# Optimization experiments

Measured on AMD Instinct MI355X. Metric: run time of the kernel, lower is better.

Reference implementation:

```python
import jax, jax.numpy as jnp
import numpy as np

B, LQ, LK, D = 32, 2048, 2048, 128
MASK_P = 0.1  # fraction of masked-out (True) positions


def setup_inputs() -> dict:
    key = jax.random.key(0)
    kq, kk, kv, km = jax.random.split(key, 4)
    q = jax.random.normal(kq, (B, LQ, D), dtype=jnp.float32)
    k = jax.random.normal(kk, (B, LK, D), dtype=jnp.float32)
    v = jax.random.normal(kv, (B, LK, D), dtype=jnp.float32)
    mask = jax.random.bernoulli(km, MASK_P, (B, LQ, LK))  # True = masked out
    return {"q": q, "k": k, "v": v, "mask": mask}


def reference(q, k, v, mask):
    # Faithful to the original: score is MULTIPLIED by sqrt(dk) (module's bug kept).
    dk = k.shape[-1]
    score = jnp.einsum('bqd,bkd->bqk', q, k) * jnp.sqrt(jnp.float32(dk))
    # masked_fill_(mask, -inf)
    score = jnp.where(mask, -jnp.inf, score)
    attn = jax.nn.softmax(score, axis=2)
    # torch.where(isnan(attn), 0, attn): fully-masked rows (all -inf) -> 0
    attn = jnp.where(jnp.isnan(attn), jnp.zeros_like(attn), attn)
    # dropout_rate = 0.0 -> identity
    context = jnp.einsum('bqk,bkd->bqd', attn, v)
    return context
```

## Files before the change

### kernel.cpp

```cpp
#include <hip/hip_runtime.h>
#include <math.h>

#define NB  32
#define NLQ 2048
#define NLK 2048
#define ND  128
#define KT  64
#define SCALE2 16.3231239813435843f
#define SCALE  11.3137084989847603904f

typedef float f32x4 __attribute__((ext_vector_type(4)));
typedef short s16x8 __attribute__((ext_vector_type(8)));
typedef unsigned short u16;
typedef unsigned short u16x8 __attribute__((ext_vector_type(8)));
typedef unsigned long long u64;

__device__ int g_maskflag;

static __device__ __forceinline__ u16 f2bf(float x) {
    unsigned int u = __float_as_uint(x);
    return (u16)((u + 0x7FFFu + ((u >> 16) & 1u)) >> 16);
}
static __device__ __forceinline__ float bf2f(u16 b) {
    return __uint_as_float(((unsigned int)b) << 16);
}

#define SPLIT8(H, L, J, VAL) do { float _v = (VAL); u16 _hb = f2bf(_v); \
    (H)[J] = (short)_hb; (L)[J] = (short)f2bf(_v - bf2f(_hb)); } while (0)

#define GLDS(lds, src) __builtin_amdgcn_global_load_lds( \
    (const __attribute__((address_space(1))) unsigned int*)(src), \
    (__attribute__((address_space(3))) unsigned int*)(lds), 16, 0, 0)

__global__ void zero_flag_kernel() { if (threadIdx.x == 0) g_maskflag = 0; }

__global__ void detect_mask_kernel(const unsigned char* __restrict__ m) {
    unsigned int i = blockIdx.x * blockDim.x + threadIdx.x;
    bool nz = m[(size_t)i * 4 + 1] != 0;
    if (__any((int)nz) && (threadIdx.x & 63) == 0) atomicOr(&g_maskflag, 1);
}

__global__ void __launch_bounds__(256)
maskbits_kernel(const unsigned char* __restrict__ M, u64* __restrict__ Bits) {
    const size_t NWORDS = (size_t)NB * NLQ * (NLK / 64);
    const int ln = threadIdx.x & 63;
    const size_t wgid = ((size_t)blockIdx.x * 256 + threadIdx.x) >> 6;
    const size_t NW = (size_t)4096 * 4;
    if (g_maskflag != 0) {
        #pragma unroll 4
        for (size_t w = wgid; w < NWORDS; w += NW) {
            unsigned char v = M[w * 64 + ln];
            u64 bal = __ballot(v != 0);
            if (ln == 0) Bits[w] = bal;
        }
    } else {
        const int* Mi = (const int*)M;
        #pragma unroll 4
        for (size_t w = wgid; w < NWORDS; w += NW) {
            int v = Mi[w * 64 + ln];
            u64 bal = __ballot(v != 0);
            if (ln == 0) Bits[w] = bal;
        }
    }
}

__global__ void __launch_bounds__(256)
ksplit_kernel(const float* __restrict__ K, u16* __restrict__ Khi, u16* __restrict__ Klo) {
    int idx  = blockIdx.x * 256 + threadIdx.x;
    int d0   = (idx & 15) << 3;
    int krow = idx >> 4;
    const float* src = K + (size_t)krow * ND + d0;
    float4 x0 = *(const float4*)src;
    float4 x1 = *(const float4*)(src + 4);
    float xs[8] = {x0.x, x0.y, x0.z, x0.w, x1.x, x1.y, x1.z, x1.w};
    u16x8 h, l;
    #pragma unroll
    for (int j = 0; j < 8; ++j) { u16 hb = f2bf(xs[j]); h[j] = hb; l[j] = f2bf(xs[j] - bf2f(hb)); }
    int kkl = krow & 63;
    size_t tbase = ((size_t)(krow >> 6)) * 8192;
    int off = (kkl * ND + d0) ^ ((kkl & 7) << 3);
    *(u16x8*)(Khi + tbase + off) = h;
    *(u16x8*)(Klo + tbase + off) = l;
}

__global__ void __launch_bounds__(256)
vtrans_kernel(const float* __restrict__ V, u16* __restrict__ Vt) {
    int gw = (blockIdx.x * 256 + threadIdx.x) >> 6;
    int ln = threadIdx.x & 63;
    int dgrp = gw & 15;
    int tile = gw >> 4;
    int dl = ln >> 3, chunk = ln & 7;
    int d = dgrp * 8 + dl;
    int kk0 = chunk * 8;
    const float* src = V + ((size_t)tile * 64 + kk0) * ND + d;
    u16x8 o;
    #pragma unroll
    for (int j = 0; j < 8; ++j) o[j] = f2bf(src[(size_t)j * ND]);
    *(u16x8*)(Vt + (size_t)tile * 8192 + ((d * KT + kk0) ^ ((d & 7) << 3))) = o;
}

__global__ void __launch_bounds__(512, 2)
attn3_kernel(const float* __restrict__ Q, const u64* __restrict__ Bits,
             float* __restrict__ Out,
             const u16* __restrict__ Khi, const u16* __restrict__ Klo,
             const u16* __restrict__ Vt)
{
    extern __shared__ u16 smem[];
    u16* bufA = smem;
    u16* bufB = smem + 24576;
    u16* sPb  = smem + 49152;

    const int tid  = threadIdx.x;
    const int wave = tid >> 6;
    const int ln   = tid & 63;
    const int g    = ln >> 4;
    const int qi   = ln & 15;

    const int n    = blockIdx.x;
    const int orig = ((n & 7) << 5) | (n >> 3);
    const int b    = orig >> 3;
    const int qt   = orig & 7;
    const int qbase = qt * 256 + wave * 32;

    s16x8 qh8[2][4], ql8[2][4];
    #pragma unroll
    for (int u = 0; u < 2; ++u) {
        const float* qp = Q + ((size_t)b * NLQ + qbase + u * 16 + qi) * ND;
        #pragma unroll
        for (int c = 0; c < 4; ++c) {
            const float* p = qp + c * 32 + g * 8;
            float4 x0 = *(const float4*)(p);
            float4 x1 = *(const float4*)(p + 4);
            s16x8 h, l;
            SPLIT8(h, l, 0, x0.x * SCALE2); SPLIT8(h, l, 1, x0.y * SCALE2);
            SPLIT8(h, l, 2, x0.z * SCALE2); SPLIT8(h, l, 3, x0.w * SCALE2);
            SPLIT8(h, l, 4, x1.x * SCALE2); SPLIT8(h, l, 5, x1.y * SCALE2);
            SPLIT8(h, l, 6, x1.z * SCALE2); SPLIT8(h, l, 7, x1.w * SCALE2);
            qh8[u][c] = h; ql8[u][c] = l;
        }
    }

    f32x4 o[2][8];
    #pragma unroll
    for (int u = 0; u < 2; ++u)
        #pragma unroll
        for (int t = 0; t < 8; ++t) o[u][t] = (f32x4){0.f, 0.f, 0.f, 0.f};
    float mrun[2] = {-INFINITY, -INFINITY}, lsum[2] = {0.f, 0.f};

    const u16* khT = Khi + (size_t)b * 32 * 8192;
    const u16* klT = Klo + (size_t)b * 32 * 8192;
    const u16* vtT = Vt  + (size_t)b * 32 * 8192;

    const size_t row0 = (size_t)b * NLQ + qbase + qi;
    const u64* bw0 = Bits + row0 * 32;
    const u64* bw1 = Bits + (row0 + 16) * 32;

#define STAGE_TILE(dst, kt_) do { \
    const char* _sK = (const char*)(khT + (size_t)(kt_) * 8192) + wave * 2048 + ln * 16; \
    const char* _sL = (const char*)(klT + (size_t)(kt_) * 8192) + wave * 2048 + ln * 16; \
    const char* _sV = (const char*)(vtT + (size_t)(kt_) * 8192) + wave * 2048 + ln * 16; \
    GLDS((dst) + wave * 1024,               _sK); \
    GLDS((dst) + wave * 1024 + 512,         _sK + 1024); \
    GLDS((dst) + 8192  + wave * 1024,       _sL); \
    GLDS((dst) + 8192  + wave * 1024 + 512, _sL + 1024); \
    GLDS((dst) + 16384 + wave * 1024,       _sV); \
    GLDS((dst) + 16384 + wave * 1024 + 512, _sV + 1024); \
} while (0)

    STAGE_TILE(bufA, 0);
    u64 mw0 = bw0[0], mw1 = bw1[0];
    __syncthreads();

    u16* cur = bufA;
    u16* nxt = bufB;

    for (int kt = 0; kt < 32; ++kt) {
        u64 nmw0 = mw0, nmw1 = mw1;
        if (kt < 31) {
            STAGE_TILE(nxt, kt + 1);
            nmw0 = bw0[kt + 1];
            nmw1 = bw1[kt + 1];
        }

        u16* sKh = cur;
        u16* sKl = cur + 8192;
        u16* sVt_ = cur + 16384;

        float p[2][16];
        #pragma unroll
        for (int s = 0; s < 4; ++s) {
            f32x4 a0 = (f32x4){0.f, 0.f, 0.f, 0.f};
            f32x4 a1 = (f32x4){0.f, 0.f, 0.f, 0.f};
            int row = s * 16 + qi;
            int rowoff = row * ND, swz = (row & 7) << 3;
            #pragma unroll
            for (int c = 0; c < 4; ++c) {
                int off = (rowoff + c * 32 + g * 8) ^ swz;
                s16x8 kh = *(s16x8*)&sKh[off];
                s16x8 kl = *(s16x8*)&sKl[off];
                a0 = __builtin_amdgcn_mfma_f32_16x16x32_bf16(kh, qh8[0][c], a0, 0, 0, 0);
                a1 = __builtin_amdgcn_mfma_f32_16x16x32_bf16(kh, qh8[1][c], a1, 0, 0, 0);
                a0 = __builtin_amdgcn_mfma_f32_16x16x32_bf16(kh, ql8[0][c], a0, 0, 0, 0);
                a1 = __builtin_amdgcn_mfma_f32_16x16x32_bf16(kh, ql8[1][c], a1, 0, 0, 0);
                a0 = __builtin_amdgcn_mfma_f32_16x16x32_bf16(kl, qh8[0][c], a0, 0, 0, 0);
                a1 = __builtin_amdgcn_mfma_f32_16x16x32_bf16(kl, qh8[1][c], a1, 0, 0, 0);
            }
            #pragma unroll
            for (int r = 0; r < 4; ++r) { p[0][s * 4 + r] = a0[r]; p[1][s * 4 + r] = a1[r]; }
        }

        #pragma unroll
        for (int u = 0; u < 2; ++u) {
            u64 mw = u ? mw1 : mw0;
            unsigned mbits = 0;
            #pragma unroll
            for (int s = 0; s < 4; ++s)
                mbits |= (unsigned)((mw >> (s * 16 + 4 * g)) & 0xFull) << (4 * s);

            float tm = -INFINITY;
            #pragma unroll
            for (int i = 0; i < 16; ++i) {
                float sv = ((mbits >> i) & 1u) ? -INFINITY : p[u][i];
                p[u][i] = sv;
                tm = fmaxf(tm, sv);
            }
            tm = fmaxf(tm, __shfl_xor(tm, 16));
            tm = fmaxf(tm, __shfl_xor(tm, 32));

            float mold = mrun[u];
            bool defer = (mold > -INFINITY) && __all((int)(tm <= mold + 8.f));
            float m_use = mold;
            if (!defer) {
                float mnew = fmaxf(mold, tm);
                float corr = (mnew == -INFINITY) ? 0.f : __builtin_exp2f(mold - mnew);
                lsum[u] *= corr;
                #pragma unroll
                for (int j = 0; j < 4; ++j) {
                    float cj = __shfl(corr, 4 * g + j, 64);
                    #pragma unroll
                    for (int t = 0; t < 8; ++t) o[u][t][j] *= cj;
                }
                mrun[u] = mnew;
                m_use = mnew;
            }

            float psum = 0.f;
            #pragma unroll
            for (int i = 0; i < 16; ++i) {
                float pv = ((mbits >> i) & 1u) ? 0.f : __builtin_exp2f(p[u][i] - m_use);
                p[u][i] = pv;
                psum += pv;
            }
            psum += __shfl_xor(psum, 16);
            psum += __shfl_xor(psum, 32);
            lsum[u] += psum;

            u16* sP = sPb + (wave * 2 + u) * 1024;
            #pragma unroll
            for (int s = 0; s < 4; ++s) {
                ushort4 p4;
                p4.x = f2bf(p[u][s * 4 + 0]); p4.y = f2bf(p[u][s * 4 + 1]);
                p4.z = f2bf(p[u][s * 4 + 2]); p4.w = f2bf(p[u][s * 4 + 3]);
                int off = (qi * KT + s * 16 + 4 * g) ^ ((qi & 7) << 3);
                *(ushort4*)&sP[off] = p4;
            }
        }

        u16* sP0 = sPb + (wave * 2 + 0) * 1024;
        u16* sP1 = sPb + (wave * 2 + 1) * 1024;
        #pragma unroll
        for (int h = 0; h < 2; ++h) {
            int offp = (qi * KT + h * 32 + g * 8) ^ ((qi & 7) << 3);
            s16x8 pa0 = *(s16x8*)&sP0[offp];
            s16x8 pa1 = *(s16x8*)&sP1[offp];
            #pragma unroll
            for (int t = 0; t < 8; ++t) {
                int d = t * 16 + qi;
                int offv = (d * KT + h * 32 + g * 8) ^ ((d & 7) << 3);
                s16x8 vb = *(s16x8*)&sVt_[offv];
                o[0][t] = __builtin_amdgcn_mfma_f32_16x16x32_bf16(pa0, vb, o[0][t], 0, 0, 0);
                o[1][t] = __builtin_amdgcn_mfma_f32_16x16x32_bf16(pa1, vb, o[1][t], 0, 0, 0);
            }
        }

        __syncthreads();
        mw0 = nmw0; mw1 = nmw1;
        u16* tswap = cur; cur = nxt; nxt = tswap;
    }

    #pragma unroll
    for (int u = 0; u < 2; ++u)
        #pragma unroll
        for (int j = 0; j < 4; ++j) {
            float lj = __shfl(lsum[u], 4 * g + j, 64);
            float inv = (lj > 0.f) ? (1.0f / lj) : 0.f;
            int row = qbase + u * 16 + 4 * g + j;
            float* op = Out + ((size_t)b * NLQ + row) * ND + qi;
            #pragma unroll
            for (int t = 0; t < 8; ++t) op[t * 16] = o[u][t][j] * inv;
        }
#undef STAGE_TILE
}

__global__ void __launch_bounds__(256, 2)
attn_fallback(const float* __restrict__ Q, const float* __restrict__ K,
              const float* __restrict__ V, const unsigned char* __restrict__ Mb,
              float* __restrict__ Out)
{
    __shared__ u16 sKh[KT * ND];
    __shared__ u16 sKl[KT * ND];
    __shared__ u16 sVt[ND * KT];
    __shared__ u16 sP[4][16 * KT];

    const int tid  = threadIdx.x;
    const int wave = tid >> 6;
    const int ln   = tid & 63;
    const int g    = ln >> 4;
    const int qi   = ln & 15;

    const int bid   = blockIdx.x;
    const int b     = bid >> 5;
    const int qt    = bid & 31;
    const int qbase = qt * 64;
    const int qrow  = qbase + wave * 16 + qi;

    const bool maskByte = (g_maskflag != 0);

    s16x8 qh8[4], ql8[4];
    {
        const float* qp = Q + ((size_t)b * NLQ + qrow) * ND;
        #pragma unroll
        for (int c = 0; c < 4; ++c) {
            const float* p = qp + c * 32 + g * 8;
            float4 x0 = *(const float4*)(p);
            float4 x1 = *(const float4*)(p + 4);
            s16x8 h, l;
            SPLIT8(h, l, 0, x0.x * SCALE); SPLIT8(h, l, 1, x0.y * SCALE);
            SPLIT8(h, l, 2, x0.z * SCALE); SPLIT8(h, l, 3, x0.w * SCALE);
            SPLIT8(h, l, 4, x1.x * SCALE); SPLIT8(h, l, 5, x1.y * SCALE);
            SPLIT8(h, l, 6, x1.z * SCALE); SPLIT8(h, l, 7, x1.w * SCALE);
            qh8[c] = h; ql8[c] = l;
        }
    }

    f32x4 o[8];
    #pragma unroll
    for (int t = 0; t < 8; ++t) o[t] = (f32x4){0.f, 0.f, 0.f, 0.f};
    float m_run = -INFINITY, lsumv = 0.f;

    const float* kbp = K + (size_t)b * NLK * ND;
    const float* vbp = V + (size_t)b * NLK * ND;
    const size_t mrow = ((size_t)b * NLQ + qrow) * (size_t)NLK;

    for (int kt = 0; kt < NLK / KT; ++kt) {
        const int kb = kt * KT;
        __syncthreads();

        #pragma unroll
        for (int r = 0; r < 8; ++r) {
            int idx = r * 256 + tid;
            int kk  = idx >> 5;
            int d0  = (idx & 31) << 2;
            float4 x = *(const float4*)(kbp + (size_t)(kb + kk) * ND + d0);
            ushort4 h4, l4; u16 hb;
            hb = f2bf(x.x); h4.x = hb; l4.x = f2bf(x.x - bf2f(hb));
            hb = f2bf(x.y); h4.y = hb; l4.y = f2bf(x.y - bf2f(hb));
            hb = f2bf(x.z); h4.z = hb; l4.z = f2bf(x.z - bf2f(hb));
            hb = f2bf(x.w); h4.w = hb; l4.w = f2bf(x.w - bf2f(hb));
            int off = (kk * ND + d0) ^ ((kk & 7) << 3);
            *(ushort4*)&sKh[off] = h4;
            *(ushort4*)&sKl[off] = l4;
        }
        #pragma unroll
        for (int r = 0; r < 2; ++r) {
            int idx = r * 256 + tid;
            int kk0 = (idx >> 5) << 2;
            int d0  = (idx & 31) << 2;
            const float* vp = vbp + (size_t)(kb + kk0) * ND + d0;
            float4 r0 = *(const float4*)(vp);
            float4 r1 = *(const float4*)(vp + ND);
            float4 r2 = *(const float4*)(vp + 2 * ND);
            float4 r3 = *(const float4*)(vp + 3 * ND);
            ushort4 cv;
            cv.x = f2bf(r0.x); cv.y = f2bf(r1.x); cv.z = f2bf(r2.x); cv.w = f2bf(r3.x);
            { int d = d0;     *(ushort4*)&sVt[(d * KT + kk0) ^ ((d & 7) << 3)] = cv; }
            cv.x = f2bf(r0.y); cv.y = f2bf(r1.y); cv.z = f2bf(r2.y); cv.w = f2bf(r3.y);
            { int d = d0 + 1; *(ushort4*)&sVt[(d * KT + kk0) ^ ((d & 7) << 3)] = cv; }
            cv.x = f2bf(r0.z); cv.y = f2bf(r1.z); cv.z = f2bf(r2.z); cv.w = f2bf(r3.z);
            { int d = d0 + 2; *(ushort4*)&sVt[(d * KT + kk0) ^ ((d & 7) << 3)] = cv; }
            cv.x = f2bf(r0.w); cv.y = f2bf(r1.w); cv.z = f2bf(r2.w); cv.w = f2bf(r3.w);
            { int d = d0 + 3; *(ushort4*)&sVt[(d * KT + kk0) ^ ((d & 7) << 3)] = cv; }
        }
        __syncthreads();

        unsigned maskbits = 0;
        if (maskByte) {
            #pragma unroll
            for (int s = 0; s < 4; ++s) {
                unsigned mm = *(const unsigned int*)(Mb + mrow + (size_t)(kb + s * 16 + 4 * g));
                #pragma unroll
                for (int j = 0; j < 4; ++j)
                    maskbits |= (((mm >> (8 * j)) & 0xFFu) ? 1u : 0u) << (s * 4 + j);
            }
        } else {
            const int* Mi = (const int*)Mb;
            #pragma unroll
            for (int s = 0; s < 4; ++s) {
                int4 mm = *(const int4*)(Mi + mrow + (size_t)(kb + s * 16 + 4 * g));
                if (mm.x) maskbits |= 1u << (s * 4 + 0);
                if (mm.y) maskbits |= 1u << (s * 4 + 1);
                if (mm.z) maskbits |= 1u << (s * 4 + 2);
                if (mm.w) maskbits |= 1u << (s * 4 + 3);
            }
        }

        float p[16];
        #pragma unroll
        for (int s = 0; s < 4; ++s) {
            f32x4 acc = (f32x4){0.f, 0.f, 0.f, 0.f};
            int rowoff = (s * 16 + qi) * ND;
            int swz = ((s * 16 + qi) & 7) << 3;
            #pragma unroll
            for (int c = 0; c < 4; ++c) {
                int off = (rowoff + c * 32 + g * 8) ^ swz;
                s16x8 kh = *(s16x8*)&sKh[off];
                s16x8 kl = *(s16x8*)&sKl[off];
                acc = __builtin_amdgcn_mfma_f32_16x16x32_bf16(kh, qh8[c], acc, 0, 0, 0);
                acc = __builtin_amdgcn_mfma_f32_16x16x32_bf16(kh, ql8[c], acc, 0, 0, 0);
                acc = __builtin_amdgcn_mfma_f32_16x16x32_bf16(kl, qh8[c], acc, 0, 0, 0);
            }
            p[s * 4 + 0] = acc[0]; p[s * 4 + 1] = acc[1];
            p[s * 4 + 2] = acc[2]; p[s * 4 + 3] = acc[3];
        }

        float tmax = -INFINITY;
        #pragma unroll
        for (int i = 0; i < 16; ++i) {
            float sv = ((maskbits >> i) & 1u) ? -INFINITY : p[i];
            p[i] = sv;
            tmax = fmaxf(tmax, sv);
        }
        tmax = fmaxf(tmax, __shfl_xor(tmax, 16));
        tmax = fmaxf(tmax, __shfl_xor(tmax, 32));
        float mnew = fmaxf(m_run, tmax);
        float corr = (mnew == -INFINITY) ? 0.f : __expf(m_run - mnew);
        float psum = 0.f;
        #pragma unroll
        for (int i = 0; i < 16; ++i) {
            float pv = ((maskbits >> i) & 1u) ? 0.f : __expf(p[i] - mnew);
            p[i] = pv;
            psum += pv;
        }
        psum += __shfl_xor(psum, 16);
        psum += __shfl_xor(psum, 32);
        lsumv = lsumv * corr + psum;
        m_run = mnew;

        #pragma unroll
        for (int j = 0; j < 4; ++j) {
            float cj = __shfl(corr, 4 * g + j, 64);
            #pragma unroll
            for (int t = 0; t < 8; ++t) o[t][j] *= cj;
        }

        #pragma unroll
        for (int s = 0; s < 4; ++s) {
            ushort4 p4;
            p4.x = f2bf(p[s * 4 + 0]); p4.y = f2bf(p[s * 4 + 1]);
            p4.z = f2bf(p[s * 4 + 2]); p4.w = f2bf(p[s * 4 + 3]);
            int off = (qi * KT + s * 16 + 4 * g) ^ ((qi & 7) << 3);
            *(ushort4*)&sP[wave][off] = p4;
        }
        #pragma unroll
        for (int h = 0; h < 2; ++h) {
            int offp = (qi * KT + h * 32 + g * 8) ^ ((qi & 7) << 3);
            s16x8 pa = *(s16x8*)&sP[wave][offp];
            #pragma unroll
            for (int t = 0; t < 8; ++t) {
                int d = t * 16 + qi;
                int offv = (d * KT + h * 32 + g * 8) ^ ((d & 7) << 3);
                s16x8 vb = *(s16x8*)&sVt[offv];
                o[t] = __builtin_amdgcn_mfma_f32_16x16x32_bf16(pa, vb, o[t], 0, 0, 0);
            }
        }
    }

    #pragma unroll
    for (int j = 0; j < 4; ++j) {
        float lj = __shfl(lsumv, 4 * g + j, 64);
        float inv = (lj > 0.f) ? (1.0f / lj) : 0.f;
        int row = qbase + wave * 16 + 4 * g + j;
        float* op = Out + ((size_t)b * NLQ + row) * ND + qi;
        #pragma unroll
        for (int t = 0; t < 8; ++t) op[t * 16] = o[t][j] * inv;
    }
}

extern "C" void kernel_launch(void* const* d_in, const int* in_sizes, int n_in,
                              void* d_out, int out_size, void* d_ws, size_t ws_size,
                              hipStream_t stream) {
    (void)in_sizes; (void)n_in; (void)out_size;
    const float* Q = (const float*)d_in[0];
    const float* K = (const float*)d_in[1];
    const float* V = (const float*)d_in[2];
    const unsigned char* M = (const unsigned char*)d_in[3];
    float* Out = (float*)d_out;

    zero_flag_kernel<<<1, 64, 0, stream>>>();
    detect_mask_kernel<<<64, 256, 0, stream>>>(M);

    const size_t WS_NEED = (size_t)64 * 1024 * 1024;
    if (ws_size >= WS_NEED) {
        u16* Khi = (u16*)d_ws;
        u16* Klo = Khi + 8388608;
        u16* Vt  = Klo + 8388608;
        u64* Bits = (u64*)(Vt + 8388608);
        maskbits_kernel<<<4096, 256, 0, stream>>>(M, Bits);
        ksplit_kernel<<<4096, 256, 0, stream>>>(K, Khi, Klo);
        vtrans_kernel<<<4096, 256, 0, stream>>>(V, Vt);
        hipFuncSetAttribute((const void*)attn3_kernel,
                            hipFuncAttributeMaxDynamicSharedMemorySize, 131072);
        attn3_kernel<<<256, 512, 131072, stream>>>(Q, Bits, Out, Khi, Klo, Vt);
    } else {
        attn_fallback<<<1024, 256, 0, stream>>>(Q, K, V, M, Out);
    }
}
```

Baseline: 964.2 us.

## Fuse prep kernels and deepen attention pipeline with LDS-staged mask bits

Merges the mask-bit, K split and V transpose kernels into a single prep launch to cut launch overhead. The attention kernel now prefetches two tiles ahead, using raw s_waitcnt/s_barrier instead of __syncthreads, and stages mask words into LDS through global_load_lds. It also interleaves the two softmax halves with the PV MFMAs and adds s_setprio around MFMA blocks to overlap compute with softmax work. Dynamic LDS grows to 144KB, and the hand-written vmcnt counts make the pipeline fragile.

```diff
diff --git a/kernel.cpp b/kernel.cpp
--- a/kernel.cpp
+++ b/kernel.cpp
@@ -41,66 +41,114 @@
 }
 
 __global__ void __launch_bounds__(256)
-maskbits_kernel(const unsigned char* __restrict__ M, u64* __restrict__ Bits) {
-    const size_t NWORDS = (size_t)NB * NLQ * (NLK / 64);
-    const int ln = threadIdx.x & 63;
-    const size_t wgid = ((size_t)blockIdx.x * 256 + threadIdx.x) >> 6;
-    const size_t NW = (size_t)4096 * 4;
-    if (g_maskflag != 0) {
-        #pragma unroll 4
-        for (size_t w = wgid; w < NWORDS; w += NW) {
-            unsigned char v = M[w * 64 + ln];
-            u64 bal = __ballot(v != 0);
-            if (ln == 0) Bits[w] = bal;
-        }
+prep_kernel(const float* __restrict__ K, const float* __restrict__ V,
+            const unsigned char* __restrict__ M,
+            u16* __restrict__ Khi, u16* __restrict__ Klo, u16* __restrict__ Vt,
+            u64* __restrict__ Bits)
+{
+    const int blk = blockIdx.x;
+    if (blk < 4096) {
+        int idx  = blk * 256 + threadIdx.x;
+        int d0   = (idx & 15) << 3;
+        int krow = idx >> 4;
+        const float* src = K + (size_t)krow * ND + d0;
+        float4 x0 = *(const float4*)src;
+        float4 x1 = *(const float4*)(src + 4);
+        float xs[8] = {x0.x, x0.y, x0.z, x0.w, x1.x, x1.y, x1.z, x1.w};
+        u16x8 h, l;
+        #pragma unroll
+        for (int j = 0; j < 8; ++j) { u16 hb = f2bf(xs[j]); h[j] = hb; l[j] = f2bf(xs[j] - bf2f(hb)); }
+        int kkl = krow & 63;
+        size_t tbase = ((size_t)(krow >> 6)) * 8192;
+        int off = (kkl * ND + d0) ^ ((kkl & 7) << 3);
+        *(u16x8*)(Khi + tbase + off) = h;
+        *(u16x8*)(Klo + tbase + off) = l;
+    } else if (blk < 8192) {
+        int gw = ((blk - 4096) * 256 + threadIdx.x) >> 6;
+        int ln = threadIdx.x & 63;
+        int dgrp = gw & 15;
+        int tile = gw >> 4;
+        int dl = ln >> 3, chunk = ln & 7;
+        int d = dgrp * 8 + dl;
+        int kk0 = chunk * 8;
+        const float* src = V + ((size_t)tile * 64 + kk0) * ND + d;
+        u16x8 ov;
+        #pragma unroll
+        for (int j = 0; j < 8; ++j) ov[j] = f2bf(src[(size_t)j * ND]);
+        *(u16x8*)(Vt + (size_t)tile * 8192 + ((d * KT + kk0) ^ ((d & 7) << 3))) = ov;
     } else {
-        const int* Mi = (const int*)M;
-        #pragma unroll 4
-        for (size_t w = wgid; w < NWORDS; w += NW) {
-            int v = Mi[w * 64 + ln];
-            u64 bal = __ballot(v != 0);
-            if (ln == 0) Bits[w] = bal;
-        }
-    }
-}
-
-__global__ void __launch_bounds__(256)
-ksplit_kernel(const float* __restrict__ K, u16* __restrict__ Khi, u16* __restrict__ Klo) {
-    int idx  = blockIdx.x * 256 + threadIdx.x;
-    int d0   = (idx & 15) << 3;
-    int krow = idx >> 4;
-    const float* src = K + (size_t)krow * ND + d0;
-    float4 x0 = *(const float4*)src;
-    float4 x1 = *(const float4*)(src + 4);
-    float xs[8] = {x0.x, x0.y, x0.z, x0.w, x1.x, x1.y, x1.z, x1.w};
-    u16x8 h, l;
-    #pragma unroll
-    for (int j = 0; j < 8; ++j) { u16 hb = f2bf(xs[j]); h[j] = hb; l[j] = f2bf(xs[j] - bf2f(hb)); }
-    int kkl = krow & 63;
-    size_t tbase = ((size_t)(krow >> 6)) * 8192;
-    int off = (kkl * ND + d0) ^ ((kkl & 7) << 3);
-    *(u16x8*)(Khi + tbase + off) = h;
-    *(u16x8*)(Klo + tbase + off) = l;
-}
-
-__global__ void __launch_bounds__(256)
-vtrans_kernel(const float* __restrict__ V, u16* __restrict__ Vt) {
-    int gw = (blockIdx.x * 256 + threadIdx.x) >> 6;
-    int ln = threadIdx.x & 63;
-    int dgrp = gw & 15;
-    int tile = gw >> 4;
-    int dl = ln >> 3, chunk = ln & 7;
-    int d = dgrp * 8 + dl;
-    int kk0 = chunk * 8;
-    const float* src = V + ((size_t)tile * 64 + kk0) * ND + d;
-    u16x8 o;
-    #pragma unroll
-    for (int j = 0; j < 8; ++j) o[j] = f2bf(src[(size_t)j * ND]);
-    *(u16x8*)(Vt + (size_t)tile * 8192 + ((d * KT + kk0) ^ ((d & 7) << 3))) = o;
-}
+        const size_t NWORDS = (size_t)NB * NLQ * (NLK / 64);
+        const int ln = threadIdx.x & 63;
+        const size_t wgid = (((size_t)(blk - 8192)) * 256 + threadIdx.x) >> 6;
+        const size_t NW = (size_t)4096 * 4;
+        if (g_maskflag != 0) {
+            #pragma unroll 4
+            for (size_t w = wgid; w < NWORDS; w += NW) {
+                unsigned char v = M[w * 64 + ln];
+                u64 bal = __ballot(v != 0);
+                if (ln == 0) Bits[w] = bal;
+            }
+        } else {
+            const int* Mi = (const int*)M;
+            #pragma unroll 4
+            for (size_t w = wgid; w < NWORDS; w += NW) {
+                int v = Mi[w * 64 + ln];
+                u64 bal = __ballot(v != 0);
+                if (ln == 0) Bits[w] = bal;
+            }
+        }
+    }
+}
+
+#define SOFTMAX_STORE(MW, P, MRUN, LSUM, OACC, SPTR) do { \
+    unsigned mbits = 0; \
+    _Pragma("unroll") \
+    for (int s = 0; s < 4; ++s) \
+        mbits |= (unsigned)(((MW) >> (s * 16 + 4 * g)) & 0xFull) << (4 * s); \
+    float tm = -INFINITY; \
+    _Pragma("unroll") \
+    for (int i = 0; i < 16; ++i) { \
+        float sv = ((mbits >> i) & 1u) ? -INFINITY : (P)[i]; \
+        (P)[i] = sv; tm = fmaxf(tm, sv); \
+    } \
+    tm = fmaxf(tm, __shfl_xor(tm, 16)); \
+    tm = fmaxf(tm, __shfl_xor(tm, 32)); \
+    float mold = (MRUN); \
+    bool defer = (mold > -INFINITY) && __all((int)(tm <= mold + 8.f)); \
+    float m_use = mold; \
+    if (!defer) { \
+        float mnew = fmaxf(mold, tm); \
+        float corr = (mnew == -INFINITY) ? 0.f : __builtin_exp2f(mold - mnew); \
+        (LSUM) *= corr; \
+        _Pragma("unroll") \
+        for (int j = 0; j < 4; ++j) { \
+            float cj = __shfl(corr, 4 * g + j, 64); \
+            _Pragma("unroll") \
+            for (int t2 = 0; t2 < 8; ++t2) (OACC)[t2][j] *= cj; \
+        } \
+        (MRUN) = mnew; m_use = mnew; \
+    } \
+    float psum = 0.f; \
+    _Pragma("unroll") \
+    for (int i = 0; i < 16; ++i) { \
+        float pv = ((mbits >> i) & 1u) ? 0.f : __builtin_exp2f((P)[i] - m_use); \
+        (P)[i] = pv; psum += pv; \
+    } \
+    psum += __shfl_xor(psum, 16); \
+    psum += __shfl_xor(psum, 32); \
+    (LSUM) += psum; \
+    _Pragma("unroll") \
+    for (int s = 0; s < 4; ++s) { \
+        ushort4 p4; \
+        p4.x = f2bf((P)[s * 4 + 0]); p4.y = f2bf((P)[s * 4 + 1]); \
+        p4.z = f2bf((P)[s * 4 + 2]); p4.w = f2bf((P)[s * 4 + 3]); \
+        int off = (qi * KT + s * 16 + 4 * g) ^ ((qi & 7) << 3); \
+        *(ushort4*)&(SPTR)[off] = p4; \
+    } \
+} while (0)
 
 __global__ void __launch_bounds__(512, 2)
-attn3_kernel(const float* __restrict__ Q, const u64* __restrict__ Bits,
+attn4_kernel(const float* __restrict__ Q, const u64* __restrict__ Bits,
              float* __restrict__ Out,
              const u16* __restrict__ Khi, const u16* __restrict__ Klo,
              const u16* __restrict__ Vt)
@@ -109,6 +157,7 @@
     u16* bufA = smem;
     u16* bufB = smem + 24576;
     u16* sPb  = smem + 49152;
+    char* mbase = (char*)(smem + 65536);
 
     const int tid  = threadIdx.x;
     const int wave = tid >> 6;
@@ -140,20 +189,16 @@
         }
     }
 
-    f32x4 o[2][8];
+    f32x4 o0[8], o1[8];
     #pragma unroll
-    for (int u = 0; u < 2; ++u)
-        #pragma unroll
-        for (int t = 0; t < 8; ++t) o[u][t] = (f32x4){0.f, 0.f, 0.f, 0.f};
-    float mrun[2] = {-INFINITY, -INFINITY}, lsum[2] = {0.f, 0.f};
+    for (int t = 0; t < 8; ++t) { o0[t] = (f32x4){0.f,0.f,0.f,0.f}; o1[t] = (f32x4){0.f,0.f,0.f,0.f}; }
+    float mrun0 = -INFINITY, mrun1 = -INFINITY, lsum0 = 0.f, lsum1 = 0.f;
 
     const u16* khT = Khi + (size_t)b * 32 * 8192;
     const u16* klT = Klo + (size_t)b * 32 * 8192;
     const u16* vtT = Vt  + (size_t)b * 32 * 8192;
-
-    const size_t row0 = (size_t)b * NLQ + qbase + qi;
-    const u64* bw0 = Bits + row0 * 32;
-    const u64* bw1 = Bits + (row0 + 16) * 32;
+    const size_t browbase = (size_t)b * NLQ + qbase;
+    char* mslotw = mbase + wave * 2048;
 
 #define STAGE_TILE(dst, kt_) do { \
     const char* _sK = (const char*)(khT + (size_t)(kt_) * 8192) + wave * 2048 + ln * 16; \
@@ -167,30 +212,40 @@
     GLDS((dst) + 16384 + wave * 1024 + 512, _sV + 1024); \
 } while (0)
 
+#define MASK_STAGE(W_) do { \
+    const char* _sm = (const char*)Bits + ((browbase + (size_t)(ln & 31)) * 32 + (size_t)(W_)) * 8; \
+    GLDS((u16*)(mslotw + (((W_) >> 1) & 1) * 1024), _sm); \
+} while (0)
+
     STAGE_TILE(bufA, 0);
-    u64 mw0 = bw0[0], mw1 = bw1[0];
-    __syncthreads();
-
-    u16* cur = bufA;
-    u16* nxt = bufB;
-
-    for (int kt = 0; kt < 32; ++kt) {
-        u64 nmw0 = mw0, nmw1 = mw1;
-        if (kt < 31) {
-            STAGE_TILE(nxt, kt + 1);
-            nmw0 = bw0[kt + 1];
-            nmw1 = bw1[kt + 1];
-        }
-
-        u16* sKh = cur;
-        u16* sKl = cur + 8192;
-        u16* sVt_ = cur + 16384;
-
-        float p[2][16];
+    MASK_STAGE(0);
+    STAGE_TILE(bufB, 1);
+    MASK_STAGE(2);
+
+    u16* sP0 = sPb + (wave * 2 + 0) * 1024;
+    u16* sP1 = sPb + (wave * 2 + 1) * 1024;
+    const int offp_h0 = (qi * KT + g * 8) ^ ((qi & 7) << 3);
+    const int offp_h1 = (qi * KT + 32 + g * 8) ^ ((qi & 7) << 3);
+
+    for (int t = 0; t < 32; ++t) {
+        u16* cbuf = (t & 1) ? bufB : bufA;
+        u16* sKh = cbuf;
+        u16* sKl = cbuf + 8192;
+        u16* sVt_ = cbuf + 16384;
+
+        asm volatile("s_waitcnt vmcnt(7)" ::: "memory");
+        asm volatile("s_barrier" ::: "memory");
+
+        const char* mbw = mslotw + ((t >> 1) & 1) * 1024 + (t & 1) * 8;
+        u64 mw0 = *(const u64*)(mbw + qi * 16);
+        u64 mw1 = *(const u64*)(mbw + 256 + qi * 16);
+
+        float p0[16], p1[16];
+        __builtin_amdgcn_s_setprio(1);
         #pragma unroll
         for (int s = 0; s < 4; ++s) {
-            f32x4 a0 = (f32x4){0.f, 0.f, 0.f, 0.f};
-            f32x4 a1 = (f32x4){0.f, 0.f, 0.f, 0.f};
+            f32x4 a0 = (f32x4){0.f,0.f,0.f,0.f};
+            f32x4 a1 = (f32x4){0.f,0.f,0.f,0.f};
             int row = s * 16 + qi;
             int rowoff = row * ND, swz = (row & 7) << 3;
             #pragma unroll
@@ -206,100 +261,80 @@
                 a1 = __builtin_amdgcn_mfma_f32_16x16x32_bf16(kl, qh8[1][c], a1, 0, 0, 0);
             }
             #pragma unroll
-            for (int r = 0; r < 4; ++r) { p[0][s * 4 + r] = a0[r]; p[1][s * 4 + r] = a1[r]; }
-        }
-
-        #pragma unroll
-        for (int u = 0; u < 2; ++u) {
-            u64 mw = u ? mw1 : mw0;
-            unsigned mbits = 0;
-            #pragma unroll
-            for (int s = 0; s < 4; ++s)
-                mbits |= (unsigned)((mw >> (s * 16 + 4 * g)) & 0xFull) << (4 * s);
-
-            float tm = -INFINITY;
-            #pragma unroll
-            for (int i = 0; i < 16; ++i) {
-                float sv = ((mbits >> i) & 1u) ? -INFINITY : p[u][i];
-                p[u][i] = sv;
-                tm = fmaxf(tm, sv);
-            }
-            tm = fmaxf(tm, __shfl_xor(tm, 16));
-            tm = fmaxf(tm, __shfl_xor(tm, 32));
-
-            float mold = mrun[u];
-            bool defer = (mold > -INFINITY) && __all((int)(tm <= mold + 8.f));
-            float m_use = mold;
-            if (!defer) {
-                float mnew = fmaxf(mold, tm);
-                float corr = (mnew == -INFINITY) ? 0.f : __builtin_exp2f(mold - mnew);
-                lsum[u] *= corr;
-                #pragma unroll
-                for (int j = 0; j < 4; ++j) {
-                    float cj = __shfl(corr, 4 * g + j, 64);
-                    #pragma unroll
-                    for (int t = 0; t < 8; ++t) o[u][t][j] *= cj;
-                }
-                mrun[u] = mnew;
-                m_use = mnew;
-            }
-
-            float psum = 0.f;
-            #pragma unroll
-            for (int i = 0; i < 16; ++i) {
-                float pv = ((mbits >> i) & 1u) ? 0.f : __builtin_exp2f(p[u][i] - m_use);
-                p[u][i] = pv;
-                psum += pv;
-            }
-            psum += __shfl_xor(psum, 16);
-            psum += __shfl_xor(psum, 32);
-            lsum[u] += psum;
-
-            u16* sP = sPb + (wave * 2 + u) * 1024;
-            #pragma unroll
-            for (int s = 0; s < 4; ++s) {
-                ushort4 p4;
-                p4.x = f2bf(p[u][s * 4 + 0]); p4.y = f2bf(p[u][s * 4 + 1]);
-                p4.z = f2bf(p[u][s * 4 + 2]); p4.w = f2bf(p[u][s * 4 + 3]);
-                int off = (qi * KT + s * 16 + 4 * g) ^ ((qi & 7) << 3);
-                *(ushort4*)&sP[off] = p4;
-            }
-        }
-
-        u16* sP0 = sPb + (wave * 2 + 0) * 1024;
-        u16* sP1 = sPb + (wave * 2 + 1) * 1024;
-        #pragma unroll
-        for (int h = 0; h < 2; ++h) {
-            int offp = (qi * KT + h * 32 + g * 8) ^ ((qi & 7) << 3);
-            s16x8 pa0 = *(s16x8*)&sP0[offp];
-            s16x8 pa1 = *(s16x8*)&sP1[offp];
-            #pragma unroll
-            for (int t = 0; t < 8; ++t) {
-                int d = t * 16 + qi;
-                int offv = (d * KT + h * 32 + g * 8) ^ ((d & 7) << 3);
-                s16x8 vb = *(s16x8*)&sVt_[offv];
-                o[0][t] = __builtin_amdgcn_mfma_f32_16x16x32_bf16(pa0, vb, o[0][t], 0, 0, 0);
-                o[1][t] = __builtin_amdgcn_mfma_f32_16x16x32_bf16(pa1, vb, o[1][t], 0, 0, 0);
-            }
-        }
-
-        __syncthreads();
-        mw0 = nmw0; mw1 = nmw1;
-        u16* tswap = cur; cur = nxt; nxt = tswap;
+            for (int r = 0; r < 4; ++r) { p0[s * 4 + r] = a0[r]; p1[s * 4 + r] = a1[r]; }
+        }
+        __builtin_amdgcn_s_setprio(0);
+
+        SOFTMAX_STORE(mw0, p0, mrun0, lsum0, o0, sP0);
+
+        s16x8 vb[8];
+        #pragma unroll
+        for (int tt = 0; tt < 8; ++tt) {
+            int d = tt * 16 + qi;
+            vb[tt] = *(s16x8*)&sVt_[(d * KT + g * 8) ^ ((d & 7) << 3)];
+        }
+        s16x8 pa00 = *(s16x8*)&sP0[offp_h0];
+        __builtin_amdgcn_s_setprio(1);
+        #pragma unroll
+        for (int tt = 0; tt < 8; ++tt)
+            o0[tt] = __builtin_amdgcn_mfma_f32_16x16x32_bf16(pa00, vb[tt], o0[tt], 0, 0, 0);
+        __builtin_amdgcn_s_setprio(0);
+
+        SOFTMAX_STORE(mw1, p1, mrun1, lsum1, o1, sP1);
+
+        s16x8 pa10 = *(s16x8*)&sP1[offp_h0];
+        __builtin_amdgcn_s_setprio(1);
+        #pragma unroll
+        for (int tt = 0; tt < 8; ++tt)
+            o1[tt] = __builtin_amdgcn_mfma_f32_16x16x32_bf16(pa10, vb[tt], o1[tt], 0, 0, 0);
+        __builtin_amdgcn_s_setprio(0);
+
+        s16x8 pa01 = *(s16x8*)&sP0[offp_h1];
+        s16x8 pa11 = *(s16x8*)&sP1[offp_h1];
+        #pragma unroll
+        for (int tt = 0; tt < 8; ++tt) {
+            int d = tt * 16 + qi;
+            vb[tt] = *(s16x8*)&sVt_[(d * KT + 32 + g * 8) ^ ((d & 7) << 3)];
+        }
+        __builtin_amdgcn_s_setprio(1);
+        #pragma unroll
+        for (int tt = 0; tt < 8; ++tt) {
+            o0[tt] = __builtin_amdgcn_mfma_f32_16x16x32_bf16(pa01, vb[tt], o0[tt], 0, 0, 0);
+            o1[tt] = __builtin_amdgcn_mfma_f32_16x16x32_bf16(pa11, vb[tt], o1[tt], 0, 0, 0);
+        }
+        __builtin_amdgcn_s_setprio(0);
+
+        asm volatile("s_waitcnt lgkmcnt(0)" ::: "memory");
+        asm volatile("s_barrier" ::: "memory");
+
+        if (t < 31) {
+            int nt = t + 2; if (nt > 31) nt = 31;
+            STAGE_TILE(cbuf, nt);
+            int W = nt & ~1; if (W > 30) W = 30;
+            MASK_STAGE(W);
+        }
     }
 
     #pragma unroll
-    for (int u = 0; u < 2; ++u)
-        #pragma unroll
-        for (int j = 0; j < 4; ++j) {
-            float lj = __shfl(lsum[u], 4 * g + j, 64);
-            float inv = (lj > 0.f) ? (1.0f / lj) : 0.f;
-            int row = qbase + u * 16 + 4 * g + j;
-            float* op = Out + ((size_t)b * NLQ + row) * ND + qi;
-            #pragma unroll
-            for (int t = 0; t < 8; ++t) op[t * 16] = o[u][t][j] * inv;
-        }
+    for (int j = 0; j < 4; ++j) {
+        float lj = __shfl(lsum0, 4 * g + j, 64);
+        float inv = (lj > 0.f) ? (1.0f / lj) : 0.f;
+        int row = qbase + 4 * g + j;
+        float* op = Out + ((size_t)b * NLQ + row) * ND + qi;
+        #pragma unroll
+        for (int tt = 0; tt < 8; ++tt) op[tt * 16] = o0[tt][j] * inv;
+    }
+    #pragma unroll
+    for (int j = 0; j < 4; ++j) {
+        float lj = __shfl(lsum1, 4 * g + j, 64);
+        float inv = (lj > 0.f) ? (1.0f / lj) : 0.f;
+        int row = qbase + 16 + 4 * g + j;
+        float* op = Out + ((size_t)b * NLQ + row) * ND + qi;
+        #pragma unroll
+        for (int tt = 0; tt < 8; ++tt) op[tt * 16] = o1[tt][j] * inv;
+    }
 #undef STAGE_TILE
+#undef MASK_STAGE
 }
 
 __global__ void __launch_bounds__(256, 2)
@@ -509,18 +544,16 @@
     zero_flag_kernel<<<1, 64, 0, stream>>>();
     detect_mask_kernel<<<64, 256, 0, stream>>>(M);
 
-    const size_t WS_NEED = (size_t)64 * 1024 * 1024;
+    const size_t WS_NEED = (size_t)64 * 1024 * 1024 + 64;
     if (ws_size >= WS_NEED) {
         u16* Khi = (u16*)d_ws;
         u16* Klo = Khi + 8388608;
         u16* Vt  = Klo + 8388608;
         u64* Bits = (u64*)(Vt + 8388608);
-        maskbits_kernel<<<4096, 256, 0, stream>>>(M, Bits);
-        ksplit_kernel<<<4096, 256, 0, stream>>>(K, Khi, Klo);
-        vtrans_kernel<<<4096, 256, 0, stream>>>(V, Vt);
-        hipFuncSetAttribute((const void*)attn3_kernel,
-                            hipFuncAttributeMaxDynamicSharedMemorySize, 131072);
-        attn3_kernel<<<256, 512, 131072, stream>>>(Q, Bits, Out, Khi, Klo, Vt);
+        prep_kernel<<<12288, 256, 0, stream>>>(K, V, M, Khi, Klo, Vt, Bits);
+        hipFuncSetAttribute((const void*)attn4_kernel,
+                            hipFuncAttributeMaxDynamicSharedMemorySize, 147456);
+        attn4_kernel<<<256, 512, 147456, stream>>>(Q, Bits, Out, Khi, Klo, Vt);
     } else {
         attn_fallback<<<1024, 256, 0, stream>>>(Q, K, V, M, Out);
     }
```

New measurement: 987.2 us. 1.02x slower.
